# Kernel optimization log

Measured on AMD Instinct MI355X. Metric: run time of the kernel, lower is better.

## Reference

```python
import jax, jax.numpy as jnp
import numpy as np

KLD_SCALE = 10.0
COMMITMENT_COST = 0.1


def setup_inputs() -> dict:
    key = jax.random.key(0)
    k1, k2 = jax.random.split(key)
    z = jax.random.normal(k1, (32, 2048, 64), dtype=jnp.float32)
    codebook = jax.random.normal(k2, (1024, 64), dtype=jnp.float32)
    return {"z": z, "codebook": codebook}


def reference(z, codebook):
    B, N, D = z.shape
    z_e = z.reshape(B * N, D)                          # (M, D)
    # squared euclidean distance: ||z||^2 - 2 z.E^T + ||E||^2
    dist = (
        jnp.sum(z_e * z_e, axis=1, keepdims=True)
        - 2.0 * (z_e @ codebook.T)
        + jnp.sum(codebook * codebook, axis=1)[None, :]
    )                                                  # (M, K)
    ind = jnp.argmin(dist, axis=1)                     # (M,)
    z_q = codebook[ind]                                # (M, D) gather
    latent_loss = (
        COMMITMENT_COST * jnp.mean((jax.lax.stop_gradient(z_q) - z_e) ** 2)
        + jnp.mean((z_q - jax.lax.stop_gradient(z_e)) ** 2)
    ) * KLD_SCALE
    # straight-through estimator
    z_q_st = z_e + jax.lax.stop_gradient(z_q - z_e)
    return z_q_st.reshape(B, N, D), latent_loss
```

## Files before the change

kernel.cpp:

```cpp
#include <hip/hip_runtime.h>
#include <hip/hip_bf16.h>
#include <float.h>

#define DIMS 64
#define KC 1024
#define M_TOTAL 65536
#define TAU 4e-3f

typedef __attribute__((ext_vector_type(8))) short bf16x8;
typedef __attribute__((ext_vector_type(4))) float f32x4;

#define SE_OFF   0
#define CTL_OFF  1024
#define PART_OFF 2048
#define PBH_OFF  4096
#define PBL_OFF  36864
#define M1_OFF   69632
#define M2_OFF   200704
#define IDX_OFF  331776

__device__ inline short f2bf(float x) {
  union { __hip_bfloat16 h; short s; } u;
  u.h = __float2bfloat16(x);
  return u.s;
}
__device__ inline float bf2f(short x) {
  union { short s; __hip_bfloat16 h; } u;
  u.s = x;
  return __bfloat162float(u.h);
}

__device__ inline void gload_lds16(const void* g, void* l) {
  __builtin_amdgcn_global_load_lds(
      (const __attribute__((address_space(1))) void*)g,
      (__attribute__((address_space(3))) void*)l, 16, 0, 0);
}

__global__ __launch_bounds__(256) void k_prep(const float* __restrict__ cb,
                                              float* __restrict__ se,
                                              unsigned int* __restrict__ ctl,
                                              unsigned short* __restrict__ pbh,
                                              unsigned short* __restrict__ pbl) {
  const int tid = blockIdx.x * 256 + threadIdx.x;
  if (tid < 4) ctl[tid] = 0;
  const int l = tid & 63;
  const int s = (tid >> 6) & 1;
  const int tt = tid >> 7;
  const int code = tt * 16 + (l & 15);
  const int k = s * 32 + (l >> 4) * 8;
  const float* p = cb + (size_t)code * DIMS + k;
  float v[8];
  ((float4*)v)[0] = ((const float4*)p)[0];
  ((float4*)v)[1] = ((const float4*)p)[1];
  bf16x8 h, lo;
#pragma unroll
  for (int j = 0; j < 8; ++j) {
    short hj = f2bf(v[j]);
    h[j] = hj;
    lo[j] = f2bf(v[j] - bf2f(hj));
  }
  *(bf16x8*)(pbh + (size_t)tid * 8) = h;
  *(bf16x8*)(pbl + (size_t)tid * 8) = lo;

  if (tid < KC) {
    const float4* q = (const float4*)(cb + (size_t)tid * DIMS);
    float a0 = 0.f, a1 = 0.f, a2 = 0.f, a3 = 0.f;
#pragma unroll
    for (int i = 0; i < DIMS / 4; ++i) {
      float4 u = q[i];
      a0 = fmaf(u.x, u.x, a0);
      a1 = fmaf(u.y, u.y, a1);
      a2 = fmaf(u.z, u.z, a2);
      a3 = fmaf(u.w, u.w, a3);
    }
    se[tid] = (a0 + a1) + (a2 + a3);
  }
}

__global__ __launch_bounds__(256, 4) void k_dist(const float* __restrict__ z,
                                                 const unsigned short* __restrict__ pbh,
                                                 const unsigned short* __restrict__ pbl,
                                                 const float* __restrict__ se,
                                                 float* __restrict__ m1o,
                                                 float* __restrict__ m2o,
                                                 int* __restrict__ idxo) {
  __shared__ bf16x8 sB[2][2][256];
  const int l = threadIdx.x & 63;
  const int w = threadIdx.x >> 6;
  const int split = blockIdx.x & 1;
  const int rb = blockIdx.x >> 1;
  const int r0 = rb * 128 + w * 32;
  const int col = l & 15;
  const int g = l >> 4;

  bf16x8 ah[2][2], al[2][2];
#pragma unroll
  for (int rs = 0; rs < 2; ++rs) {
    const float* zp = z + (size_t)(r0 + rs * 16 + col) * DIMS + g * 8;
#pragma unroll
    for (int ks = 0; ks < 2; ++ks) {
      float v[8];
      ((float4*)v)[0] = ((const float4*)(zp + ks * 32))[0];
      ((float4*)v)[1] = ((const float4*)(zp + ks * 32))[1];
#pragma unroll
      for (int j = 0; j < 8; ++j) {
        short hj = f2bf(v[j]);
        ah[rs][ks][j] = hj;
        al[rs][ks][j] = f2bf(v[j] - bf2f(hj));
      }
    }
  }

  float m1[2][4], m2[2][4];
  int bt[2][4];
#pragma unroll
  for (int rs = 0; rs < 2; ++rs)
#pragma unroll
    for (int j = 0; j < 4; ++j) {
      m1[rs][j] = FLT_MAX;
      m2[rs][j] = FLT_MAX;
      bt[rs][j] = 0;
    }

  const int cg0 = split * 16;
  {
    const size_t f = (size_t)cg0 * 256 + w * 64 + l;
    gload_lds16(pbh + f * 8, &sB[0][0][w * 64]);
    gload_lds16(pbl + f * 8, &sB[0][1][w * 64]);
  }
  __syncthreads();

  int cur = 0;
  for (int c = 0; c < 16; ++c) {
    if (c + 1 < 16) {
      const size_t f = (size_t)(cg0 + c + 1) * 256 + w * 64 + l;
      gload_lds16(pbh + f * 8, &sB[cur ^ 1][0][w * 64]);
      gload_lds16(pbl + f * 8, &sB[cur ^ 1][1][w * 64]);
    }
#pragma unroll
    for (int tt = 0; tt < 2; ++tt) {
      const int gt = cg0 * 2 + c * 2 + tt;
      bf16x8 bh0 = sB[cur][0][tt * 128 + l];
      bf16x8 bh1 = sB[cur][0][tt * 128 + 64 + l];
      bf16x8 bl0 = sB[cur][1][tt * 128 + l];
      bf16x8 bl1 = sB[cur][1][tt * 128 + 64 + l];
      const float sec = se[gt * 16 + col];
      f32x4 acc0 = {0.f, 0.f, 0.f, 0.f};
      f32x4 acc1 = {0.f, 0.f, 0.f, 0.f};
      acc0 = __builtin_amdgcn_mfma_f32_16x16x32_bf16(ah[0][0], bh0, acc0, 0, 0, 0);
      acc1 = __builtin_amdgcn_mfma_f32_16x16x32_bf16(ah[1][0], bh0, acc1, 0, 0, 0);
      acc0 = __builtin_amdgcn_mfma_f32_16x16x32_bf16(ah[0][1], bh1, acc0, 0, 0, 0);
      acc1 = __builtin_amdgcn_mfma_f32_16x16x32_bf16(ah[1][1], bh1, acc1, 0, 0, 0);
      acc0 = __builtin_amdgcn_mfma_f32_16x16x32_bf16(ah[0][0], bl0, acc0, 0, 0, 0);
      acc1 = __builtin_amdgcn_mfma_f32_16x16x32_bf16(ah[1][0], bl0, acc1, 0, 0, 0);
      acc0 = __builtin_amdgcn_mfma_f32_16x16x32_bf16(ah[0][1], bl1, acc0, 0, 0, 0);
      acc1 = __builtin_amdgcn_mfma_f32_16x16x32_bf16(ah[1][1], bl1, acc1, 0, 0, 0);
      acc0 = __builtin_amdgcn_mfma_f32_16x16x32_bf16(al[0][0], bh0, acc0, 0, 0, 0);
      acc1 = __builtin_amdgcn_mfma_f32_16x16x32_bf16(al[1][0], bh0, acc1, 0, 0, 0);
      acc0 = __builtin_amdgcn_mfma_f32_16x16x32_bf16(al[0][1], bh1, acc0, 0, 0, 0);
      acc1 = __builtin_amdgcn_mfma_f32_16x16x32_bf16(al[1][1], bh1, acc1, 0, 0, 0);
#pragma unroll
      for (int rs = 0; rs < 2; ++rs) {
        const f32x4 acc = rs ? acc1 : acc0;
#pragma unroll
        for (int j = 0; j < 4; ++j) {
          float d = fmaf(-2.f, acc[j], sec);
          float nm2 = __builtin_amdgcn_fmed3f(d, m1[rs][j], m2[rs][j]);
          bool lt = d < m1[rs][j];
          m1[rs][j] = lt ? d : m1[rs][j];
          bt[rs][j] = lt ? gt : bt[rs][j];
          m2[rs][j] = nm2;
        }
      }
    }
    __syncthreads();
    cur ^= 1;
  }

#pragma unroll
  for (int rs = 0; rs < 2; ++rs)
#pragma unroll
    for (int j = 0; j < 4; ++j) {
      float m1j = m1[rs][j], m2j = m2[rs][j];
      int ij = bt[rs][j] * 16 + col;
      for (int msk = 1; msk <= 8; msk <<= 1) {
        float o1 = __shfl_xor(m1j, msk);
        float o2 = __shfl_xor(m2j, msk);
        int oi = __shfl_xor(ij, msk);
        bool take = (o1 < m1j) || (o1 == m1j && oi < ij);
        float hi = take ? m1j : o1;
        m2j = fminf(fminf(m2j, o2), hi);
        m1j = take ? o1 : m1j;
        ij = take ? oi : ij;
      }
      if (col == 0) {
        const int o = split * M_TOTAL + r0 + rs * 16 + g * 4 + j;
        m1o[o] = m1j;
        m2o[o] = m2j;
        idxo[o] = ij;
      }
    }
}

__global__ __launch_bounds__(256) void k_merge(const float* __restrict__ m1s,
                                               const float* __restrict__ m2s,
                                               int* __restrict__ idxs,
                                               int* __restrict__ wl,
                                               unsigned int* __restrict__ ctl) {
  const int row = blockIdx.x * 256 + threadIdx.x;
  const float a1 = m1s[row], b1 = m1s[M_TOTAL + row];
  const float a2 = m2s[row], b2 = m2s[M_TOTAL + row];
  const int ia = idxs[row], ib = idxs[M_TOTAL + row];
  const float m1 = fminf(a1, b1);
  const float m2 = fminf(fmaxf(a1, b1), fminf(a2, b2));
  idxs[row] = (b1 < a1) ? ib : ia;
  if (m2 - m1 < TAU) {
    int p = atomicAdd((int*)ctl, 1);
    wl[p] = row;
  }
}

__global__ __launch_bounds__(256) void k_refine(const float* __restrict__ z,
                                                const float* __restrict__ cb,
                                                const int* __restrict__ wl,
                                                const unsigned int* __restrict__ ctl,
                                                int* __restrict__ idxo) {
  __shared__ float zz[64];
  __shared__ double sd[256];
  __shared__ int si[256];
  const int t = threadIdx.x;
  const int n = (int)ctl[0];
  for (int wi = blockIdx.x; wi < n; wi += 1024) {
    const int row = wl[wi];
    if (t < 16) ((float4*)zz)[t] = ((const float4*)(z + (size_t)row * DIMS))[t];
    __syncthreads();
    const int c0 = t * 4;
    double accd[4] = {0.0, 0.0, 0.0, 0.0};
    for (int ch = 0; ch < 4; ++ch) {
      float zr[16];
#pragma unroll
      for (int q = 0; q < 4; ++q) ((float4*)zr)[q] = ((float4*)zz)[ch * 4 + q];
#pragma unroll
      for (int cc = 0; cc < 4; ++cc) {
        const float* e = cb + (size_t)(c0 + cc) * DIMS + ch * 16;
#pragma unroll
        for (int q = 0; q < 16; ++q) {
          double df = (double)zr[q] - (double)e[q];
          accd[cc] = fma(df, df, accd[cc]);
        }
      }
    }
    double best = 1e300;
    int bi = 0;
#pragma unroll
    for (int cc = 0; cc < 4; ++cc)
      if (accd[cc] < best) { best = accd[cc]; bi = c0 + cc; }
    sd[t] = best;
    si[t] = bi;
    __syncthreads();
    for (int off = 128; off > 0; off >>= 1) {
      if (t < off) {
        double ob = sd[t + off];
        int oi = si[t + off];
        if (ob < sd[t] || (ob == sd[t] && oi < si[t])) { sd[t] = ob; si[t] = oi; }
      }
      __syncthreads();
    }
    if (t == 0) idxo[row] = si[0];
    __syncthreads();
  }
}

__global__ __launch_bounds__(256) void k_out(const float* __restrict__ z,
                                             const float* __restrict__ cb,
                                             const int* __restrict__ idxi,
                                             float* __restrict__ out,
                                             float* __restrict__ partials) {
  const int tid = blockIdx.x * 256 + threadIdx.x;
  const int row = tid >> 2;
  const int q = tid & 3;
  const int code = idxi[row];
  const float4* zp = (const float4*)(z + (size_t)row * DIMS + q * 16);
  const float4* ep = (const float4*)(cb + (size_t)code * DIMS + q * 16);
  float4* op = (float4*)(out + (size_t)row * DIMS + q * 16);
  float sse = 0.f;
#pragma unroll
  for (int i = 0; i < 4; ++i) {
    float4 v = zp[i], e = ep[i];
    float dx = e.x - v.x, dy = e.y - v.y, dz = e.z - v.z, dw = e.w - v.w;
    sse = fmaf(dx, dx, sse);
    sse = fmaf(dy, dy, sse);
    sse = fmaf(dz, dz, sse);
    sse = fmaf(dw, dw, sse);
    float4 o;
    o.x = v.x + dx;
    o.y = v.y + dy;
    o.z = v.z + dz;
    o.w = v.w + dw;
    op[i] = o;
  }
  __shared__ float sh[256];
  sh[threadIdx.x] = sse;
  __syncthreads();
  for (int off = 128; off > 0; off >>= 1) {
    if (threadIdx.x < off) sh[threadIdx.x] += sh[threadIdx.x + off];
    __syncthreads();
  }
  if (threadIdx.x == 0) partials[blockIdx.x] = sh[0];
}

__global__ __launch_bounds__(256) void k_loss(const float* __restrict__ partials,
                                              float* __restrict__ out) {
  __shared__ float sh[256];
  const int t = threadIdx.x;
  sh[t] = partials[t] + partials[t + 256] + partials[t + 512] + partials[t + 768];
  __syncthreads();
  for (int off = 128; off > 0; off >>= 1) {
    if (t < off) sh[t] += sh[t + off];
    __syncthreads();
  }
  if (t == 0) {
    out[(size_t)M_TOTAL * DIMS] = sh[0] * (11.0f / (float)((size_t)M_TOTAL * DIMS));
  }
}

extern "C" void kernel_launch(void* const* d_in, const int* in_sizes, int n_in,
                              void* d_out, int out_size, void* d_ws, size_t ws_size,
                              hipStream_t stream) {
  const float* z = (const float*)d_in[0];
  const float* cb = (const float*)d_in[1];
  float* out = (float*)d_out;
  float* ws = (float*)d_ws;

  float* se = ws + SE_OFF;
  unsigned int* ctl = (unsigned int*)(ws + CTL_OFF);
  float* partials = ws + PART_OFF;
  unsigned short* pbh = (unsigned short*)(ws + PBH_OFF);
  unsigned short* pbl = (unsigned short*)(ws + PBL_OFF);
  float* m1s = ws + M1_OFF;
  float* m2s = ws + M2_OFF;
  int* idx = (int*)(ws + IDX_OFF);
  int* wl = (int*)(ws + PBH_OFF);

  k_prep<<<32, 256, 0, stream>>>(cb, se, ctl, pbh, pbl);
  k_dist<<<(M_TOTAL / 128) * 2, 256, 0, stream>>>(z, pbh, pbl, se, m1s, m2s, idx);
  k_merge<<<M_TOTAL / 256, 256, 0, stream>>>(m1s, m2s, idx, wl, ctl);
  k_refine<<<1024, 256, 0, stream>>>(z, cb, wl, ctl, idx);
  k_out<<<M_TOTAL / 64, 256, 0, stream>>>(z, cb, idx, out, partials);
  k_loss<<<1, 256, 0, stream>>>(partials, out);
}
```

Before: 64.38 us.

## Split codebook four ways and stage each slice fully in LDS

The distance kernel now uses 512-thread blocks covering 256 rows each, with the codebook split into four 256-entry slices instead of two 512-entry halves. Each block loads its whole bf16 hi/lo slice and the matching squared norms into LDS once, which removes the double-buffered loop and its per-chunk barriers. The merge kernel is generalised to fold four per-split top-2 results. In exchange each z row is converted to bf16 four times instead of twice, partial-result traffic doubles, and the 64KB LDS per block limits how many blocks fit on a CU.

```diff
diff --git a/kernel.cpp b/kernel.cpp
--- a/kernel.cpp
+++ b/kernel.cpp
@@ -6,6 +6,8 @@
 #define KC 1024
 #define M_TOTAL 65536
 #define TAU 4e-3f
+#define NSPLIT 4
+#define CPS 256
 
 typedef __attribute__((ext_vector_type(8))) short bf16x8;
 typedef __attribute__((ext_vector_type(4))) float f32x4;
@@ -16,8 +18,8 @@
 #define PBH_OFF  4096
 #define PBL_OFF  36864
 #define M1_OFF   69632
-#define M2_OFF   200704
-#define IDX_OFF  331776
+#define M2_OFF   331776
+#define IDX_OFF  593920
 
 __device__ inline short f2bf(float x) {
   union { __hip_bfloat16 h; short s; } u;
@@ -77,21 +79,32 @@
   }
 }
 
-__global__ __launch_bounds__(256, 4) void k_dist(const float* __restrict__ z,
+__global__ __launch_bounds__(512, 4) void k_dist(const float* __restrict__ z,
                                                  const unsigned short* __restrict__ pbh,
                                                  const unsigned short* __restrict__ pbl,
                                                  const float* __restrict__ se,
                                                  float* __restrict__ m1o,
                                                  float* __restrict__ m2o,
                                                  int* __restrict__ idxo) {
-  __shared__ bf16x8 sB[2][2][256];
+  __shared__ bf16x8 sBH[2048];
+  __shared__ bf16x8 sBL[2048];
+  __shared__ float sSE[CPS];
   const int l = threadIdx.x & 63;
   const int w = threadIdx.x >> 6;
-  const int split = blockIdx.x & 1;
-  const int rb = blockIdx.x >> 1;
-  const int r0 = rb * 128 + w * 32;
+  const int split = blockIdx.x & 3;
+  const int rg = blockIdx.x >> 2;
+  const int r0 = rg * 256 + w * 32;
   const int col = l & 15;
   const int g = l >> 4;
+
+  const size_t pbase = (size_t)split * 2048;
+#pragma unroll
+  for (int it = 0; it < 4; ++it) {
+    const size_t f = pbase + it * 512 + w * 64 + l;
+    gload_lds16(pbh + f * 8, &sBH[it * 512 + w * 64]);
+    gload_lds16(pbl + f * 8, &sBL[it * 512 + w * 64]);
+  }
+  if (w == 0) gload_lds16(se + split * CPS + l * 4, &sSE[0]);
 
   bf16x8 ah[2][2], al[2][2];
 #pragma unroll
@@ -122,59 +135,42 @@
       bt[rs][j] = 0;
     }
 
-  const int cg0 = split * 16;
-  {
-    const size_t f = (size_t)cg0 * 256 + w * 64 + l;
-    gload_lds16(pbh + f * 8, &sB[0][0][w * 64]);
-    gload_lds16(pbl + f * 8, &sB[0][1][w * 64]);
-  }
   __syncthreads();
 
-  int cur = 0;
-  for (int c = 0; c < 16; ++c) {
-    if (c + 1 < 16) {
-      const size_t f = (size_t)(cg0 + c + 1) * 256 + w * 64 + l;
-      gload_lds16(pbh + f * 8, &sB[cur ^ 1][0][w * 64]);
-      gload_lds16(pbl + f * 8, &sB[cur ^ 1][1][w * 64]);
-    }
-#pragma unroll
-    for (int tt = 0; tt < 2; ++tt) {
-      const int gt = cg0 * 2 + c * 2 + tt;
-      bf16x8 bh0 = sB[cur][0][tt * 128 + l];
-      bf16x8 bh1 = sB[cur][0][tt * 128 + 64 + l];
-      bf16x8 bl0 = sB[cur][1][tt * 128 + l];
-      bf16x8 bl1 = sB[cur][1][tt * 128 + 64 + l];
-      const float sec = se[gt * 16 + col];
-      f32x4 acc0 = {0.f, 0.f, 0.f, 0.f};
-      f32x4 acc1 = {0.f, 0.f, 0.f, 0.f};
-      acc0 = __builtin_amdgcn_mfma_f32_16x16x32_bf16(ah[0][0], bh0, acc0, 0, 0, 0);
-      acc1 = __builtin_amdgcn_mfma_f32_16x16x32_bf16(ah[1][0], bh0, acc1, 0, 0, 0);
-      acc0 = __builtin_amdgcn_mfma_f32_16x16x32_bf16(ah[0][1], bh1, acc0, 0, 0, 0);
-      acc1 = __builtin_amdgcn_mfma_f32_16x16x32_bf16(ah[1][1], bh1, acc1, 0, 0, 0);
-      acc0 = __builtin_amdgcn_mfma_f32_16x16x32_bf16(ah[0][0], bl0, acc0, 0, 0, 0);
-      acc1 = __builtin_amdgcn_mfma_f32_16x16x32_bf16(ah[1][0], bl0, acc1, 0, 0, 0);
-      acc0 = __builtin_amdgcn_mfma_f32_16x16x32_bf16(ah[0][1], bl1, acc0, 0, 0, 0);
-      acc1 = __builtin_amdgcn_mfma_f32_16x16x32_bf16(ah[1][1], bl1, acc1, 0, 0, 0);
-      acc0 = __builtin_amdgcn_mfma_f32_16x16x32_bf16(al[0][0], bh0, acc0, 0, 0, 0);
-      acc1 = __builtin_amdgcn_mfma_f32_16x16x32_bf16(al[1][0], bh0, acc1, 0, 0, 0);
-      acc0 = __builtin_amdgcn_mfma_f32_16x16x32_bf16(al[0][1], bh1, acc0, 0, 0, 0);
-      acc1 = __builtin_amdgcn_mfma_f32_16x16x32_bf16(al[1][1], bh1, acc1, 0, 0, 0);
-#pragma unroll
-      for (int rs = 0; rs < 2; ++rs) {
-        const f32x4 acc = rs ? acc1 : acc0;
-#pragma unroll
-        for (int j = 0; j < 4; ++j) {
-          float d = fmaf(-2.f, acc[j], sec);
-          float nm2 = __builtin_amdgcn_fmed3f(d, m1[rs][j], m2[rs][j]);
-          bool lt = d < m1[rs][j];
-          m1[rs][j] = lt ? d : m1[rs][j];
-          bt[rs][j] = lt ? gt : bt[rs][j];
-          m2[rs][j] = nm2;
-        }
-      }
-    }
-    __syncthreads();
-    cur ^= 1;
+#pragma unroll 4
+  for (int tt = 0; tt < 16; ++tt) {
+    bf16x8 bh0 = sBH[tt * 128 + l];
+    bf16x8 bh1 = sBH[tt * 128 + 64 + l];
+    bf16x8 bl0 = sBL[tt * 128 + l];
+    bf16x8 bl1 = sBL[tt * 128 + 64 + l];
+    const float sec = sSE[tt * 16 + col];
+    f32x4 acc0 = {0.f, 0.f, 0.f, 0.f};
+    f32x4 acc1 = {0.f, 0.f, 0.f, 0.f};
+    acc0 = __builtin_amdgcn_mfma_f32_16x16x32_bf16(ah[0][0], bh0, acc0, 0, 0, 0);
+    acc1 = __builtin_amdgcn_mfma_f32_16x16x32_bf16(ah[1][0], bh0, acc1, 0, 0, 0);
+    acc0 = __builtin_amdgcn_mfma_f32_16x16x32_bf16(ah[0][1], bh1, acc0, 0, 0, 0);
+    acc1 = __builtin_amdgcn_mfma_f32_16x16x32_bf16(ah[1][1], bh1, acc1, 0, 0, 0);
+    acc0 = __builtin_amdgcn_mfma_f32_16x16x32_bf16(ah[0][0], bl0, acc0, 0, 0, 0);
+    acc1 = __builtin_amdgcn_mfma_f32_16x16x32_bf16(ah[1][0], bl0, acc1, 0, 0, 0);
+    acc0 = __builtin_amdgcn_mfma_f32_16x16x32_bf16(ah[0][1], bl1, acc0, 0, 0, 0);
+    acc1 = __builtin_amdgcn_mfma_f32_16x16x32_bf16(ah[1][1], bl1, acc1, 0, 0, 0);
+    acc0 = __builtin_amdgcn_mfma_f32_16x16x32_bf16(al[0][0], bh0, acc0, 0, 0, 0);
+    acc1 = __builtin_amdgcn_mfma_f32_16x16x32_bf16(al[1][0], bh0, acc1, 0, 0, 0);
+    acc0 = __builtin_amdgcn_mfma_f32_16x16x32_bf16(al[0][1], bh1, acc0, 0, 0, 0);
+    acc1 = __builtin_amdgcn_mfma_f32_16x16x32_bf16(al[1][1], bh1, acc1, 0, 0, 0);
+#pragma unroll
+    for (int rs = 0; rs < 2; ++rs) {
+      const f32x4 acc = rs ? acc1 : acc0;
+#pragma unroll
+      for (int j = 0; j < 4; ++j) {
+        float d = fmaf(-2.f, acc[j], sec);
+        float nm2 = __builtin_amdgcn_fmed3f(d, m1[rs][j], m2[rs][j]);
+        bool lt = d < m1[rs][j];
+        m1[rs][j] = lt ? d : m1[rs][j];
+        bt[rs][j] = lt ? tt : bt[rs][j];
+        m2[rs][j] = nm2;
+      }
+    }
   }
 
 #pragma unroll
@@ -182,7 +178,7 @@
 #pragma unroll
     for (int j = 0; j < 4; ++j) {
       float m1j = m1[rs][j], m2j = m2[rs][j];
-      int ij = bt[rs][j] * 16 + col;
+      int ij = split * CPS + bt[rs][j] * 16 + col;
       for (int msk = 1; msk <= 8; msk <<= 1) {
         float o1 = __shfl_xor(m1j, msk);
         float o2 = __shfl_xor(m2j, msk);
@@ -208,12 +204,22 @@
                                                int* __restrict__ wl,
                                                unsigned int* __restrict__ ctl) {
   const int row = blockIdx.x * 256 + threadIdx.x;
-  const float a1 = m1s[row], b1 = m1s[M_TOTAL + row];
-  const float a2 = m2s[row], b2 = m2s[M_TOTAL + row];
-  const int ia = idxs[row], ib = idxs[M_TOTAL + row];
-  const float m1 = fminf(a1, b1);
-  const float m2 = fminf(fmaxf(a1, b1), fminf(a2, b2));
-  idxs[row] = (b1 < a1) ? ib : ia;
+  float m1 = FLT_MAX, m2 = FLT_MAX;
+  int bi = 0;
+#pragma unroll
+  for (int s = 0; s < NSPLIT; ++s) {
+    const float a1 = m1s[s * M_TOTAL + row];
+    const float a2 = m2s[s * M_TOTAL + row];
+    const int ai = idxs[s * M_TOTAL + row];
+    if (a1 < m1) {
+      m2 = fminf(m1, a2);
+      m1 = a1;
+      bi = ai;
+    } else {
+      m2 = fminf(m2, a1);
+    }
+  }
+  idxs[row] = bi;
   if (m2 - m1 < TAU) {
     int p = atomicAdd((int*)ctl, 1);
     wl[p] = row;
@@ -343,7 +349,7 @@
   int* wl = (int*)(ws + PBH_OFF);
 
   k_prep<<<32, 256, 0, stream>>>(cb, se, ctl, pbh, pbl);
-  k_dist<<<(M_TOTAL / 128) * 2, 256, 0, stream>>>(z, pbh, pbl, se, m1s, m2s, idx);
+  k_dist<<<(M_TOTAL / 256) * NSPLIT, 512, 0, stream>>>(z, pbh, pbl, se, m1s, m2s, idx);
   k_merge<<<M_TOTAL / 256, 256, 0, stream>>>(m1s, m2s, idx, wl, ctl);
   k_refine<<<1024, 256, 0, stream>>>(z, cb, wl, ctl, idx);
   k_out<<<M_TOTAL / 64, 256, 0, stream>>>(z, cb, idx, out, partials);
```

New measurement: 69.47 us. 1.08x slower.

## Switch distance kernel to 32x32x16 bf16 MFMA with single accumulator tile

Applied to the files above, without the earlier changes.

Replaces the 16x16x32 MFMA tiling (two 16-row tiles per wave, two code tiles per chunk) with one 32x32x16 MFMA tile per wave per chunk, changing the codebook pre-pack layout in k_prep to match. Each lane now tracks 16 rows' min/second-min state and the cross-lane reduction spans 32 lanes. The worklist buffer moves to its own workspace offset instead of aliasing the packed codebook. This aims to cut MFMA issue count and per-tile overhead (se loads, LDS reads), at the cost of more registers for 16-element accumulators and tracking state.

```diff
diff --git a/kernel.cpp b/kernel.cpp
--- a/kernel.cpp
+++ b/kernel.cpp
@@ -8,7 +8,7 @@
 #define TAU 4e-3f
 
 typedef __attribute__((ext_vector_type(8))) short bf16x8;
-typedef __attribute__((ext_vector_type(4))) float f32x4;
+typedef __attribute__((ext_vector_type(16))) float f32x16;
 
 #define SE_OFF   0
 #define CTL_OFF  1024
@@ -18,6 +18,7 @@
 #define M1_OFF   69632
 #define M2_OFF   200704
 #define IDX_OFF  331776
+#define WL_OFF   462848
 
 __device__ inline short f2bf(float x) {
   union { __hip_bfloat16 h; short s; } u;
@@ -44,10 +45,10 @@
   const int tid = blockIdx.x * 256 + threadIdx.x;
   if (tid < 4) ctl[tid] = 0;
   const int l = tid & 63;
-  const int s = (tid >> 6) & 1;
-  const int tt = tid >> 7;
-  const int code = tt * 16 + (l & 15);
-  const int k = s * 32 + (l >> 4) * 8;
+  const int s = (tid >> 6) & 3;
+  const int t = tid >> 8;
+  const int code = t * 32 + (l & 31);
+  const int k = s * 16 + (l >> 5) * 8;
   const float* p = cb + (size_t)code * DIMS + k;
   float v[8];
   ((float4*)v)[0] = ((const float4*)p)[0];
@@ -76,6 +77,27 @@
     se[tid] = (a0 + a1) + (a2 + a3);
   }
 }
+
+__device__ inline void loadA(const float* zp, bf16x8& h, bf16x8& lo) {
+  float v[8];
+  ((float4*)v)[0] = ((const float4*)zp)[0];
+  ((float4*)v)[1] = ((const float4*)zp)[1];
+#pragma unroll
+  for (int j = 0; j < 8; ++j) {
+    short hj = f2bf(v[j]);
+    h[j] = hj;
+    lo[j] = f2bf(v[j] - bf2f(hj));
+  }
+}
+
+#define UPD(dv, m1v, m2v, btv)                        \
+  {                                                   \
+    float d_ = (dv);                                  \
+    m2v = __builtin_amdgcn_fmed3f(d_, m1v, m2v);      \
+    bool lt_ = d_ < m1v;                              \
+    m1v = lt_ ? d_ : m1v;                             \
+    btv = lt_ ? c : btv;                              \
+  }
 
 __global__ __launch_bounds__(256, 4) void k_dist(const float* __restrict__ z,
                                                  const unsigned short* __restrict__ pbh,
@@ -90,41 +112,26 @@
   const int split = blockIdx.x & 1;
   const int rb = blockIdx.x >> 1;
   const int r0 = rb * 128 + w * 32;
-  const int col = l & 15;
-  const int g = l >> 4;
-
-  bf16x8 ah[2][2], al[2][2];
-#pragma unroll
-  for (int rs = 0; rs < 2; ++rs) {
-    const float* zp = z + (size_t)(r0 + rs * 16 + col) * DIMS + g * 8;
-#pragma unroll
-    for (int ks = 0; ks < 2; ++ks) {
-      float v[8];
-      ((float4*)v)[0] = ((const float4*)(zp + ks * 32))[0];
-      ((float4*)v)[1] = ((const float4*)(zp + ks * 32))[1];
-#pragma unroll
-      for (int j = 0; j < 8; ++j) {
-        short hj = f2bf(v[j]);
-        ah[rs][ks][j] = hj;
-        al[rs][ks][j] = f2bf(v[j] - bf2f(hj));
-      }
-    }
-  }
-
-  float m1[2][4], m2[2][4];
-  int bt[2][4];
-#pragma unroll
-  for (int rs = 0; rs < 2; ++rs)
-#pragma unroll
-    for (int j = 0; j < 4; ++j) {
-      m1[rs][j] = FLT_MAX;
-      m2[rs][j] = FLT_MAX;
-      bt[rs][j] = 0;
-    }
-
-  const int cg0 = split * 16;
+  const int rr = l & 31;
+  const int g = l >> 5;
+
+  const float* zrow = z + (size_t)(r0 + rr) * DIMS + g * 8;
+  bf16x8 ah[4], al[4];
+#pragma unroll
+  for (int s = 0; s < 4; ++s) loadA(zrow + s * 16, ah[s], al[s]);
+
+  float m1[16], m2[16];
+  int bt[16];
+#pragma unroll
+  for (int j = 0; j < 16; ++j) {
+    m1[j] = FLT_MAX;
+    m2[j] = FLT_MAX;
+    bt[j] = 0;
+  }
+
+  const int T0 = split * 16;
   {
-    const size_t f = (size_t)cg0 * 256 + w * 64 + l;
+    const size_t f = (size_t)T0 * 256 + w * 64 + l;
     gload_lds16(pbh + f * 8, &sB[0][0][w * 64]);
     gload_lds16(pbl + f * 8, &sB[0][1][w * 64]);
   }
@@ -133,73 +140,51 @@
   int cur = 0;
   for (int c = 0; c < 16; ++c) {
     if (c + 1 < 16) {
-      const size_t f = (size_t)(cg0 + c + 1) * 256 + w * 64 + l;
+      const size_t f = (size_t)(T0 + c + 1) * 256 + w * 64 + l;
       gload_lds16(pbh + f * 8, &sB[cur ^ 1][0][w * 64]);
       gload_lds16(pbl + f * 8, &sB[cur ^ 1][1][w * 64]);
     }
-#pragma unroll
-    for (int tt = 0; tt < 2; ++tt) {
-      const int gt = cg0 * 2 + c * 2 + tt;
-      bf16x8 bh0 = sB[cur][0][tt * 128 + l];
-      bf16x8 bh1 = sB[cur][0][tt * 128 + 64 + l];
-      bf16x8 bl0 = sB[cur][1][tt * 128 + l];
-      bf16x8 bl1 = sB[cur][1][tt * 128 + 64 + l];
-      const float sec = se[gt * 16 + col];
-      f32x4 acc0 = {0.f, 0.f, 0.f, 0.f};
-      f32x4 acc1 = {0.f, 0.f, 0.f, 0.f};
-      acc0 = __builtin_amdgcn_mfma_f32_16x16x32_bf16(ah[0][0], bh0, acc0, 0, 0, 0);
-      acc1 = __builtin_amdgcn_mfma_f32_16x16x32_bf16(ah[1][0], bh0, acc1, 0, 0, 0);
-      acc0 = __builtin_amdgcn_mfma_f32_16x16x32_bf16(ah[0][1], bh1, acc0, 0, 0, 0);
-      acc1 = __builtin_amdgcn_mfma_f32_16x16x32_bf16(ah[1][1], bh1, acc1, 0, 0, 0);
-      acc0 = __builtin_amdgcn_mfma_f32_16x16x32_bf16(ah[0][0], bl0, acc0, 0, 0, 0);
-      acc1 = __builtin_amdgcn_mfma_f32_16x16x32_bf16(ah[1][0], bl0, acc1, 0, 0, 0);
-      acc0 = __builtin_amdgcn_mfma_f32_16x16x32_bf16(ah[0][1], bl1, acc0, 0, 0, 0);
-      acc1 = __builtin_amdgcn_mfma_f32_16x16x32_bf16(ah[1][1], bl1, acc1, 0, 0, 0);
-      acc0 = __builtin_amdgcn_mfma_f32_16x16x32_bf16(al[0][0], bh0, acc0, 0, 0, 0);
-      acc1 = __builtin_amdgcn_mfma_f32_16x16x32_bf16(al[1][0], bh0, acc1, 0, 0, 0);
-      acc0 = __builtin_amdgcn_mfma_f32_16x16x32_bf16(al[0][1], bh1, acc0, 0, 0, 0);
-      acc1 = __builtin_amdgcn_mfma_f32_16x16x32_bf16(al[1][1], bh1, acc1, 0, 0, 0);
-#pragma unroll
-      for (int rs = 0; rs < 2; ++rs) {
-        const f32x4 acc = rs ? acc1 : acc0;
-#pragma unroll
-        for (int j = 0; j < 4; ++j) {
-          float d = fmaf(-2.f, acc[j], sec);
-          float nm2 = __builtin_amdgcn_fmed3f(d, m1[rs][j], m2[rs][j]);
-          bool lt = d < m1[rs][j];
-          m1[rs][j] = lt ? d : m1[rs][j];
-          bt[rs][j] = lt ? gt : bt[rs][j];
-          m2[rs][j] = nm2;
-        }
-      }
+    const float sec = se[(T0 + c) * 32 + rr];
+    f32x16 acc = {0.f, 0.f, 0.f, 0.f, 0.f, 0.f, 0.f, 0.f,
+                  0.f, 0.f, 0.f, 0.f, 0.f, 0.f, 0.f, 0.f};
+#pragma unroll
+    for (int s = 0; s < 4; ++s) {
+      bf16x8 bh = sB[cur][0][s * 64 + l];
+      bf16x8 bl = sB[cur][1][s * 64 + l];
+      acc = __builtin_amdgcn_mfma_f32_32x32x16_bf16(ah[s], bh, acc, 0, 0, 0);
+      acc = __builtin_amdgcn_mfma_f32_32x32x16_bf16(ah[s], bl, acc, 0, 0, 0);
+      acc = __builtin_amdgcn_mfma_f32_32x32x16_bf16(al[s], bh, acc, 0, 0, 0);
+    }
+#pragma unroll
+    for (int j = 0; j < 16; ++j) {
+      UPD(fmaf(-2.f, acc[j], sec), m1[j], m2[j], bt[j]);
     }
     __syncthreads();
     cur ^= 1;
   }
 
 #pragma unroll
-  for (int rs = 0; rs < 2; ++rs)
-#pragma unroll
-    for (int j = 0; j < 4; ++j) {
-      float m1j = m1[rs][j], m2j = m2[rs][j];
-      int ij = bt[rs][j] * 16 + col;
-      for (int msk = 1; msk <= 8; msk <<= 1) {
-        float o1 = __shfl_xor(m1j, msk);
-        float o2 = __shfl_xor(m2j, msk);
-        int oi = __shfl_xor(ij, msk);
-        bool take = (o1 < m1j) || (o1 == m1j && oi < ij);
-        float hi = take ? m1j : o1;
-        m2j = fminf(fminf(m2j, o2), hi);
-        m1j = take ? o1 : m1j;
-        ij = take ? oi : ij;
-      }
-      if (col == 0) {
-        const int o = split * M_TOTAL + r0 + rs * 16 + g * 4 + j;
-        m1o[o] = m1j;
-        m2o[o] = m2j;
-        idxo[o] = ij;
-      }
-    }
+  for (int j = 0; j < 16; ++j) {
+    float m1j = m1[j], m2j = m2[j];
+    int ij = split * 512 + bt[j] * 32 + rr;
+    for (int msk = 1; msk <= 16; msk <<= 1) {
+      float o1 = __shfl_xor(m1j, msk);
+      float o2 = __shfl_xor(m2j, msk);
+      int oi = __shfl_xor(ij, msk);
+      bool take = (o1 < m1j) || (o1 == m1j && oi < ij);
+      float hi = take ? m1j : o1;
+      m2j = fminf(fminf(m2j, o2), hi);
+      m1j = take ? o1 : m1j;
+      ij = take ? oi : ij;
+    }
+    if (rr == 0) {
+      const int row = r0 + (j & 3) + 8 * (j >> 2) + 4 * g;
+      const int o = split * M_TOTAL + row;
+      m1o[o] = m1j;
+      m2o[o] = m2j;
+      idxo[o] = ij;
+    }
+  }
 }
 
 __global__ __launch_bounds__(256) void k_merge(const float* __restrict__ m1s,
@@ -340,7 +325,7 @@
   float* m1s = ws + M1_OFF;
   float* m2s = ws + M2_OFF;
   int* idx = (int*)(ws + IDX_OFF);
-  int* wl = (int*)(ws + PBH_OFF);
+  int* wl = (int*)(ws + WL_OFF);
 
   k_prep<<<32, 256, 0, stream>>>(cb, se, ctl, pbh, pbl);
   k_dist<<<(M_TOTAL / 128) * 2, 256, 0, stream>>>(z, pbh, pbl, se, m1s, m2s, idx);
```

Result: slower. 71.22 us (+10.6%).
